# Optimization experiments

Measured on AMD Instinct MI355X. Metric: run time of the kernel, lower is better.

## Reference

```python
import jax, jax.numpy as jnp
import numpy as np

N_NODES = 50000
N_EDGES = 600000
D = 128
R = 8


def setup_inputs() -> dict:
    key = jax.random.key(0)
    ks = jax.random.split(key, 10)
    return {
        "node_ids": jnp.arange(N_NODES, dtype=jnp.int32),
        "src": jax.random.randint(ks[0], (N_EDGES,), 0, N_NODES, dtype=jnp.int32),
        "dst": jax.random.randint(ks[1], (N_EDGES,), 0, N_NODES, dtype=jnp.int32),
        "etype": jax.random.randint(ks[2], (N_EDGES,), 0, R, dtype=jnp.int32),
        "emb": jax.random.normal(ks[3], (N_NODES, D), dtype=jnp.float32) * 0.02,
        "W1": jax.random.normal(ks[4], (R, D, D), dtype=jnp.float32) * 0.05,
        "Wself1": jax.random.normal(ks[5], (D, D), dtype=jnp.float32) * 0.05,
        "b1": jnp.zeros((D,), dtype=jnp.float32),
        "W2": jax.random.normal(ks[6], (R, D, D), dtype=jnp.float32) * 0.05,
        "Wself2": jax.random.normal(ks[7], (D, D), dtype=jnp.float32) * 0.05,
        "b2": jnp.zeros((D,), dtype=jnp.float32),
    }


def rgcn_layer(h, W, Wself, b, src, dst, etype, n_nodes):
    # relation-wise transform of all node features: [R, N, d_out]
    hr = jnp.einsum('nd,rdo->rno', h, W)
    # per-edge gather of (relation, src) -> message, then scatter-sum to dst
    msgs = hr[etype, src]                                   # [E, d_out]
    agg = jax.ops.segment_sum(msgs, dst, num_segments=n_nodes)
    # self-loop + bias (activation=None, feat_drop=0)
    return agg + h @ Wself + b


def reference(node_ids, src, dst, etype, emb, W1, Wself1, b1, W2, Wself2, b2):
    h0 = emb[node_ids]                                      # embedding lookup over all nodes
    h1 = rgcn_layer(h0, W1, Wself1, b1, src, dst, etype, emb.shape[0])
    h2 = rgcn_layer(h1, W2, Wself2, b2, src, dst, etype, emb.shape[0])
    return h2
```

## Files before the change

kernel.cpp:

```cpp
#include <hip/hip_runtime.h>
#include <hip/hip_bf16.h>

#define NN 50000
#define NE 600000
#define DD 128
#define NR 8
#define NB (NN * NR)
#define NCHUNK8 ((NB + 255) / 256)
#define PERT ((NCHUNK8 + 255) / 256)
#define CAPE 1024

typedef __attribute__((ext_vector_type(8))) short bf16x8;
typedef __attribute__((ext_vector_type(4))) float f32x4;

__device__ __forceinline__ unsigned short f2bf(float f) {
  __hip_bfloat16 h = __float2bfloat16(f);
  return *reinterpret_cast<unsigned short*>(&h);
}
__device__ __forceinline__ unsigned pk2(float lo, float hi) {
  return (unsigned)f2bf(lo) | ((unsigned)f2bf(hi) << 16);
}
__device__ __forceinline__ float bflo(unsigned u) { return __uint_as_float(u << 16); }
__device__ __forceinline__ float bfhi(unsigned u) { return __uint_as_float(u & 0xffff0000u); }

__global__ __launch_bounds__(256) void convw_kernel(
    const float* __restrict__ W1, const float* __restrict__ Ws1,
    const float* __restrict__ W2, const float* __restrict__ Ws2,
    unsigned short* __restrict__ WT)
{
  __shared__ float tile[16][17];
  const int m = blockIdx.y;
  const int t8 = blockIdx.x;
  const int d0 = (t8 >> 3) * 16, o0 = (t8 & 7) * 16;
  const float* src;
  if (m < 8)       src = W1 + (size_t)m * DD * DD;
  else if (m == 8) src = Ws1;
  else if (m < 17) src = W2 + (size_t)(m - 9) * DD * DD;
  else             src = Ws2;
  const int tx = threadIdx.x & 15, ty = threadIdx.x >> 4;
  tile[ty][tx] = src[(size_t)(d0 + ty) * DD + o0 + tx];
  __syncthreads();
  WT[(size_t)m * DD * DD + (o0 + ty) * DD + d0 + tx] = f2bf(tile[tx][ty]);
}

__global__ __launch_bounds__(256) void convh_kernel(
    const float* __restrict__ emb, const int* __restrict__ ids,
    unsigned short* __restrict__ h)
{
  const int gid = blockIdx.x * 256 + threadIdx.x;
  if (gid >= NN * 16) return;
  const int row = gid >> 4;
  const int off = (gid & 15) * 8;
  const int srcRow = ids[row];
  const float* src = emb + (size_t)srcRow * DD + off;
  const float4 a = *reinterpret_cast<const float4*>(src);
  const float4 b = *reinterpret_cast<const float4*>(src + 4);
  uint4 u;
  u.x = pk2(a.x, a.y); u.y = pk2(a.z, a.w);
  u.z = pk2(b.x, b.y); u.w = pk2(b.z, b.w);
  *reinterpret_cast<uint4*>(h + (size_t)row * DD + off) = u;
}

__global__ __launch_bounds__(256) void hist_kernel(
    const int* __restrict__ dst, const int* __restrict__ et,
    int* __restrict__ deg)
{
  const int e = blockIdx.x * 256 + threadIdx.x;
  if (e < NE) atomicAdd(&deg[dst[e] * NR + et[e]], 1);
}

__global__ __launch_bounds__(256) void bsum_kernel(
    const int* __restrict__ deg, int* __restrict__ bsum)
{
  __shared__ int tmp[256];
  const int t = threadIdx.x;
  const int i = blockIdx.x * 256 + t;
  tmp[t] = (i < NB) ? deg[i] : 0;
  __syncthreads();
#pragma unroll
  for (int off = 128; off > 0; off >>= 1) {
    if (t < off) tmp[t] += tmp[t + off];
    __syncthreads();
  }
  if (t == 0) bsum[blockIdx.x] = tmp[0];
}

__global__ __launch_bounds__(256) void bscan_kernel(
    const int* __restrict__ bsum, int* __restrict__ bbase)
{
  __shared__ int tmp[256];
  const int t = threadIdx.x;
  const int b = t * PERT;
  const int e = min(b + PERT, NCHUNK8);
  int s = 0;
  for (int i = b; i < e; ++i) s += bsum[i];
  tmp[t] = s;
  __syncthreads();
#pragma unroll
  for (int off = 1; off < 256; off <<= 1) {
    const int x = (t >= off) ? tmp[t - off] : 0;
    __syncthreads();
    tmp[t] += x;
    __syncthreads();
  }
  int run = tmp[t] - s;
  for (int i = b; i < e; ++i) {
    const int v = bsum[i];
    bbase[i] = run;
    run += v;
  }
}

__global__ __launch_bounds__(256) void expand_kernel(
    int* deg, const int* __restrict__ bbase, int* __restrict__ offsets)
{
  __shared__ int tmp[256];
  const int t = threadIdx.x;
  const int i = blockIdx.x * 256 + t;
  const int v = (i < NB) ? deg[i] : 0;
  tmp[t] = v;
  __syncthreads();
#pragma unroll
  for (int off = 1; off < 256; off <<= 1) {
    const int x = (t >= off) ? tmp[t - off] : 0;
    __syncthreads();
    tmp[t] += x;
    __syncthreads();
  }
  const int base = bbase[blockIdx.x];
  const int excl = base + tmp[t] - v;
  if (i < NB) {
    offsets[i] = excl;
    deg[i] = excl;
    if (i == NB - 1) offsets[NB] = base + tmp[t];
  }
}

__global__ __launch_bounds__(256) void fill_kernel(
    const int* __restrict__ src, const int* __restrict__ dst,
    const int* __restrict__ et, int* __restrict__ cursor,
    int* __restrict__ eidx)
{
  const int e = blockIdx.x * 256 + threadIdx.x;
  if (e < NE) {
    const int pos = atomicAdd(&cursor[dst[e] * NR + et[e]], 1);
    eidx[pos] = src[e];
  }
}

__device__ __forceinline__ void gather_frag_lds(
    const unsigned short* __restrict__ h,
    const int* __restrict__ eidx, const int* ldsE, int blockBeg,
    int beg, int end, int g, bf16x8* frag)
{
  float s[4][8];
#pragma unroll
  for (int ks = 0; ks < 4; ++ks)
#pragma unroll
    for (int j = 0; j < 8; ++j) s[ks][j] = 0.f;
  for (int i = beg; i < end; ++i) {
    const int li = i - blockBeg;
    const int idx = (li < CAPE) ? ldsE[li] : eidx[i];
    const unsigned short* hp = h + (size_t)idx * DD + g * 8;
#pragma unroll
    for (int ks = 0; ks < 4; ++ks) {
      const uint4 q = *reinterpret_cast<const uint4*>(hp + ks * 32);
      s[ks][0] += bflo(q.x); s[ks][1] += bfhi(q.x);
      s[ks][2] += bflo(q.y); s[ks][3] += bfhi(q.y);
      s[ks][4] += bflo(q.z); s[ks][5] += bfhi(q.z);
      s[ks][6] += bflo(q.w); s[ks][7] += bfhi(q.w);
    }
  }
#pragma unroll
  for (int ks = 0; ks < 4; ++ks) {
    uint4 u;
    u.x = pk2(s[ks][0], s[ks][1]);
    u.y = pk2(s[ks][2], s[ks][3]);
    u.z = pk2(s[ks][4], s[ks][5]);
    u.w = pk2(s[ks][6], s[ks][7]);
    frag[ks] = *reinterpret_cast<bf16x8*>(&u);
  }
}

template<int OUTF32>
__global__ __launch_bounds__(256, 4) void layer_kernel(
    const unsigned short* __restrict__ h,
    const int* __restrict__ off8, const int* __restrict__ eidx,
    const unsigned short* __restrict__ WTl,
    const float* __restrict__ bias,
    void* __restrict__ out)
{
  __shared__ __align__(16) char ldsW[2][DD * 64 * 2];
  __shared__ int ldsO[64 * NR + 1];
  __shared__ int ldsE[CAPE];

  const int tid = threadIdx.x;
  const int rowBase = blockIdx.x * 64;
  const int lane = tid & 63;
  const int w = tid >> 6;
  const int c = lane & 15;
  const int g = lane >> 4;
  const int n = rowBase + w * 16 + c;
  const int nld = (n < NN) ? n : (NN - 1);
  const int lnode = nld - rowBase;

  const int nNodes = (NN - rowBase < 64) ? (NN - rowBase) : 64;
  const int onum = nNodes * NR + 1;
  for (int i = tid; i < onum; i += 256) ldsO[i] = off8[rowBase * NR + i];
  __syncthreads();
  const int blockBeg = ldsO[0];
  const int blockCnt = ldsO[onum - 1] - blockBeg;
  const int stCnt = (blockCnt < CAPE) ? blockCnt : CAPE;
  for (int i = tid; i < stCnt; i += 256) ldsE[i] = eidx[blockBeg + i];

  int dstB[4], srcRel[4];
#pragma unroll
  for (int j = 0; j < 4; ++j) {
    const int i = tid + j * 256;
    const int o = i >> 3, slot = i & 7;
    dstB[j] = ((o << 7) | (slot << 4)) ^ ((o & 7) << 4);
    srcRel[j] = o * DD + slot * 8;
  }

  uint4 wreg[4];
#pragma unroll
  for (int j = 0; j < 4; ++j)
    wreg[j] = *reinterpret_cast<const uint4*>(WTl + srcRel[j]);
#pragma unroll
  for (int j = 0; j < 4; ++j)
    *reinterpret_cast<uint4*>(ldsW[0] + dstB[j]) = wreg[j];
  __syncthreads();

  bf16x8 fA[4], fB[4];
  gather_frag_lds(h, eidx, ldsE, blockBeg, ldsO[lnode * NR], ldsO[lnode * NR + 1], g, fA);

  f32x4 acc[8];
#pragma unroll
  for (int t = 0; t < 8; ++t) acc[t] = (f32x4){0.f, 0.f, 0.f, 0.f};

#define PH(P, CUR, NXT)                                                               \
  {                                                                                   \
    __syncthreads();                                                                  \
    if ((P) < 17) {                                                                   \
      const unsigned short* wsrc = WTl                                                \
          + (size_t)(((P) + 1) >> 1) * DD * DD + (((P) + 1) & 1) * 64;                \
      _Pragma("unroll")                                                               \
      for (int j = 0; j < 4; ++j)                                                     \
        wreg[j] = *reinterpret_cast<const uint4*>(wsrc + srcRel[j]);                  \
    }                                                                                 \
    int gb = 0, ge = 0;                                                               \
    if (((P) & 1) == 0 && ((P) >> 1) + 1 < NR) {                                      \
      const int lo = lnode * NR + ((P) >> 1) + 1;                                     \
      gb = ldsO[lo]; ge = ldsO[lo + 1];                                               \
    }                                                                                 \
    _Pragma("unroll")                                                                 \
    for (int kl = 0; kl < 2; ++kl) {                                                  \
      _Pragma("unroll")                                                               \
      for (int t = 0; t < 8; ++t) {                                                   \
        const int addr = (((t * 16 + c) << 7) + ((kl * 4 + g) << 4)) ^ ((c & 7) << 4); \
        bf16x8 a = *reinterpret_cast<const bf16x8*>(ldsW[(P) & 1] + addr);            \
        acc[t] = __builtin_amdgcn_mfma_f32_16x16x32_bf16(                             \
            a, CUR[((P) & 1) * 2 + kl], acc[t], 0, 0, 0);                             \
      }                                                                               \
    }                                                                                 \
    if (((P) & 1) == 0) {                                                             \
      if (((P) >> 1) + 1 < NR) {                                                      \
        gather_frag_lds(h, eidx, ldsE, blockBeg, gb, ge, g, NXT);                     \
      } else if (((P) >> 1) + 1 == NR) {                                              \
        _Pragma("unroll")                                                             \
        for (int ks = 0; ks < 4; ++ks)                                                \
          NXT[ks] = *reinterpret_cast<const bf16x8*>(                                 \
              h + (size_t)nld * DD + ks * 32 + g * 8);                                \
      }                                                                               \
    }                                                                                 \
    if ((P) < 17) {                                                                   \
      _Pragma("unroll")                                                               \
      for (int j = 0; j < 4; ++j)                                                     \
        *reinterpret_cast<uint4*>(ldsW[((P) + 1) & 1] + dstB[j]) = wreg[j];           \
    }                                                                                 \
  }

  PH(0, fA, fB)  PH(1, fA, fB)
  PH(2, fB, fA)  PH(3, fB, fA)
  PH(4, fA, fB)  PH(5, fA, fB)
  PH(6, fB, fA)  PH(7, fB, fA)
  PH(8, fA, fB)  PH(9, fA, fB)
  PH(10, fB, fA) PH(11, fB, fA)
  PH(12, fA, fB) PH(13, fA, fB)
  PH(14, fB, fA) PH(15, fB, fA)
  PH(16, fA, fB) PH(17, fA, fB)
#undef PH

  if (n >= NN) return;
  if (OUTF32) {
    float* dst = (float*)out + (size_t)n * DD;
#pragma unroll
    for (int t = 0; t < 8; ++t) {
      const int o0 = t * 16 + g * 4;
      const float4 bv = *reinterpret_cast<const float4*>(bias + o0);
      float4 o;
      o.x = acc[t][0] + bv.x; o.y = acc[t][1] + bv.y;
      o.z = acc[t][2] + bv.z; o.w = acc[t][3] + bv.w;
      *reinterpret_cast<float4*>(dst + o0) = o;
    }
  } else {
    unsigned short* dst = (unsigned short*)out + (size_t)n * DD;
#pragma unroll
    for (int t = 0; t < 8; ++t) {
      const int o0 = t * 16 + g * 4;
      const float4 bv = *reinterpret_cast<const float4*>(bias + o0);
      uint2 q;
      q.x = pk2(acc[t][0] + bv.x, acc[t][1] + bv.y);
      q.y = pk2(acc[t][2] + bv.z, acc[t][3] + bv.w);
      *reinterpret_cast<uint2*>(dst + o0) = q;
    }
  }
}

extern "C" void kernel_launch(void* const* d_in, const int* in_sizes, int n_in,
                              void* d_out, int out_size, void* d_ws, size_t ws_size,
                              hipStream_t stream) {
  const int*   node_ids = (const int*)d_in[0];
  const int*   src   = (const int*)d_in[1];
  const int*   dst   = (const int*)d_in[2];
  const int*   etype = (const int*)d_in[3];
  const float* emb   = (const float*)d_in[4];
  const float* W1    = (const float*)d_in[5];
  const float* Ws1   = (const float*)d_in[6];
  const float* b1    = (const float*)d_in[7];
  const float* W2    = (const float*)d_in[8];
  const float* Ws2   = (const float*)d_in[9];
  const float* b2    = (const float*)d_in[10];

  char* p = (char*)d_ws;
  unsigned short* h0 = (unsigned short*)p;  p += (size_t)NN * DD * 2;
  unsigned short* h1 = (unsigned short*)p;  p += (size_t)NN * DD * 2;
  unsigned short* WT = (unsigned short*)p;  p += (size_t)18 * DD * DD * 2;
  int* off8          = (int*)p;             p += (size_t)(NB + 1) * 4;
  int* deg8          = (int*)p;             p += (size_t)NB * 4;
  int* eidx          = (int*)p;             p += (size_t)NE * 4;
  int* bsum          = (int*)p;             p += (size_t)NCHUNK8 * 4;
  int* bbase         = (int*)p;

  const int eb = (NE + 255) / 256;
  const int tb = (NN + 63) / 64;

  convw_kernel<<<dim3(64, 18), 256, 0, stream>>>(W1, Ws1, W2, Ws2, WT);
  convh_kernel<<<(NN * 16) / 256, 256, 0, stream>>>(emb, node_ids, h0);
  hipMemsetAsync(deg8, 0, (size_t)NB * 4, stream);
  hist_kernel<<<eb, 256, 0, stream>>>(dst, etype, deg8);
  bsum_kernel<<<NCHUNK8, 256, 0, stream>>>(deg8, bsum);
  bscan_kernel<<<1, 256, 0, stream>>>(bsum, bbase);
  expand_kernel<<<NCHUNK8, 256, 0, stream>>>(deg8, bbase, off8);
  fill_kernel<<<eb, 256, 0, stream>>>(src, dst, etype, deg8, eidx);

  layer_kernel<0><<<tb, 256, 0, stream>>>(h0, off8, eidx, WT, b1, h1);
  layer_kernel<1><<<tb, 256, 0, stream>>>(h1, off8, eidx, WT + (size_t)9 * DD * DD, b2, (float*)d_out);
}
```

Before: 238.4 us.

## Fuse CSR build and conversion kernels into one cooperative grid-sync kernel

```diff
diff --git a/kernel.cpp b/kernel.cpp
--- a/kernel.cpp
+++ b/kernel.cpp
@@ -1,5 +1,8 @@
 #include <hip/hip_runtime.h>
 #include <hip/hip_bf16.h>
+#include <hip/hip_cooperative_groups.h>
+
+namespace cg = cooperative_groups;
 
 #define NN 50000
 #define NE 600000
@@ -9,6 +12,7 @@
 #define NCHUNK8 ((NB + 255) / 256)
 #define PERT ((NCHUNK8 + 255) / 256)
 #define CAPE 1024
+#define COOPB 1024
 
 typedef __attribute__((ext_vector_type(8))) short bf16x8;
 typedef __attribute__((ext_vector_type(4))) float f32x4;
@@ -23,128 +27,129 @@
 __device__ __forceinline__ float bflo(unsigned u) { return __uint_as_float(u << 16); }
 __device__ __forceinline__ float bfhi(unsigned u) { return __uint_as_float(u & 0xffff0000u); }
 
-__global__ __launch_bounds__(256) void convw_kernel(
+__global__ __launch_bounds__(256) void csr_coop_kernel(
     const float* __restrict__ W1, const float* __restrict__ Ws1,
     const float* __restrict__ W2, const float* __restrict__ Ws2,
-    unsigned short* __restrict__ WT)
+    const float* __restrict__ emb, const int* __restrict__ ids,
+    const int* __restrict__ srcA, const int* __restrict__ dstA,
+    const int* __restrict__ etA,
+    unsigned short* __restrict__ WT, unsigned short* __restrict__ h0,
+    int* deg, int* off8, int* __restrict__ eidx,
+    int* __restrict__ bsum, int* __restrict__ bbase)
 {
+  cg::grid_group grid = cg::this_grid();
   __shared__ float tile[16][17];
-  const int m = blockIdx.y;
-  const int t8 = blockIdx.x;
-  const int d0 = (t8 >> 3) * 16, o0 = (t8 & 7) * 16;
-  const float* src;
-  if (m < 8)       src = W1 + (size_t)m * DD * DD;
-  else if (m == 8) src = Ws1;
-  else if (m < 17) src = W2 + (size_t)(m - 9) * DD * DD;
-  else             src = Ws2;
-  const int tx = threadIdx.x & 15, ty = threadIdx.x >> 4;
-  tile[ty][tx] = src[(size_t)(d0 + ty) * DD + o0 + tx];
-  __syncthreads();
-  WT[(size_t)m * DD * DD + (o0 + ty) * DD + d0 + tx] = f2bf(tile[tx][ty]);
-}
-
-__global__ __launch_bounds__(256) void convh_kernel(
-    const float* __restrict__ emb, const int* __restrict__ ids,
-    unsigned short* __restrict__ h)
-{
-  const int gid = blockIdx.x * 256 + threadIdx.x;
-  if (gid >= NN * 16) return;
-  const int row = gid >> 4;
-  const int off = (gid & 15) * 8;
-  const int srcRow = ids[row];
-  const float* src = emb + (size_t)srcRow * DD + off;
-  const float4 a = *reinterpret_cast<const float4*>(src);
-  const float4 b = *reinterpret_cast<const float4*>(src + 4);
-  uint4 u;
-  u.x = pk2(a.x, a.y); u.y = pk2(a.z, a.w);
-  u.z = pk2(b.x, b.y); u.w = pk2(b.z, b.w);
-  *reinterpret_cast<uint4*>(h + (size_t)row * DD + off) = u;
-}
-
-__global__ __launch_bounds__(256) void hist_kernel(
-    const int* __restrict__ dst, const int* __restrict__ et,
-    int* __restrict__ deg)
-{
-  const int e = blockIdx.x * 256 + threadIdx.x;
-  if (e < NE) atomicAdd(&deg[dst[e] * NR + et[e]], 1);
-}
-
-__global__ __launch_bounds__(256) void bsum_kernel(
-    const int* __restrict__ deg, int* __restrict__ bsum)
-{
   __shared__ int tmp[256];
+
   const int t = threadIdx.x;
-  const int i = blockIdx.x * 256 + t;
-  tmp[t] = (i < NB) ? deg[i] : 0;
-  __syncthreads();
-#pragma unroll
-  for (int off = 128; off > 0; off >>= 1) {
-    if (t < off) tmp[t] += tmp[t + off];
-    __syncthreads();
-  }
-  if (t == 0) bsum[blockIdx.x] = tmp[0];
-}
-
-__global__ __launch_bounds__(256) void bscan_kernel(
-    const int* __restrict__ bsum, int* __restrict__ bbase)
-{
-  __shared__ int tmp[256];
-  const int t = threadIdx.x;
-  const int b = t * PERT;
-  const int e = min(b + PERT, NCHUNK8);
-  int s = 0;
-  for (int i = b; i < e; ++i) s += bsum[i];
-  tmp[t] = s;
-  __syncthreads();
-#pragma unroll
-  for (int off = 1; off < 256; off <<= 1) {
-    const int x = (t >= off) ? tmp[t - off] : 0;
-    __syncthreads();
-    tmp[t] += x;
-    __syncthreads();
-  }
-  int run = tmp[t] - s;
-  for (int i = b; i < e; ++i) {
-    const int v = bsum[i];
-    bbase[i] = run;
-    run += v;
-  }
-}
-
-__global__ __launch_bounds__(256) void expand_kernel(
-    int* deg, const int* __restrict__ bbase, int* __restrict__ offsets)
-{
-  __shared__ int tmp[256];
-  const int t = threadIdx.x;
-  const int i = blockIdx.x * 256 + t;
-  const int v = (i < NB) ? deg[i] : 0;
-  tmp[t] = v;
-  __syncthreads();
-#pragma unroll
-  for (int off = 1; off < 256; off <<= 1) {
-    const int x = (t >= off) ? tmp[t - off] : 0;
-    __syncthreads();
-    tmp[t] += x;
-    __syncthreads();
-  }
-  const int base = bbase[blockIdx.x];
-  const int excl = base + tmp[t] - v;
-  if (i < NB) {
-    offsets[i] = excl;
-    deg[i] = excl;
-    if (i == NB - 1) offsets[NB] = base + tmp[t];
-  }
-}
-
-__global__ __launch_bounds__(256) void fill_kernel(
-    const int* __restrict__ src, const int* __restrict__ dst,
-    const int* __restrict__ et, int* __restrict__ cursor,
-    int* __restrict__ eidx)
-{
-  const int e = blockIdx.x * 256 + threadIdx.x;
-  if (e < NE) {
-    const int pos = atomicAdd(&cursor[dst[e] * NR + et[e]], 1);
-    eidx[pos] = src[e];
+  const int b = blockIdx.x;
+  const int nthr = COOPB * 256;
+  const int gid0 = b * 256 + t;
+  const int tx = t & 15, ty = t >> 4;
+
+  for (int tileId = b; tileId < 18 * 64; tileId += COOPB) {
+    const int m = tileId >> 6, t8 = tileId & 63;
+    const int d0 = (t8 >> 3) * 16, o0 = (t8 & 7) * 16;
+    const float* sw;
+    if (m < 8)       sw = W1 + (size_t)m * DD * DD;
+    else if (m == 8) sw = Ws1;
+    else if (m < 17) sw = W2 + (size_t)(m - 9) * DD * DD;
+    else             sw = Ws2;
+    __syncthreads();
+    tile[ty][tx] = sw[(size_t)(d0 + ty) * DD + o0 + tx];
+    __syncthreads();
+    WT[(size_t)m * DD * DD + (o0 + ty) * DD + d0 + tx] = f2bf(tile[tx][ty]);
+  }
+
+  for (int gid = gid0; gid < NN * 16; gid += nthr) {
+    const int row = gid >> 4;
+    const int off = (gid & 15) * 8;
+    const int srcRow = ids[row];
+    const float* s = emb + (size_t)srcRow * DD + off;
+    const float4 a = *reinterpret_cast<const float4*>(s);
+    const float4 c = *reinterpret_cast<const float4*>(s + 4);
+    uint4 u;
+    u.x = pk2(a.x, a.y); u.y = pk2(a.z, a.w);
+    u.z = pk2(c.x, c.y); u.w = pk2(c.z, c.w);
+    *reinterpret_cast<uint4*>(h0 + (size_t)row * DD + off) = u;
+  }
+
+  for (int i = gid0; i < NB; i += nthr) deg[i] = 0;
+
+  grid.sync();
+
+  for (int e = gid0; e < NE; e += nthr)
+    atomicAdd(&deg[dstA[e] * NR + etA[e]], 1);
+
+  grid.sync();
+
+  for (int ch = b; ch < NCHUNK8; ch += COOPB) {
+    const int i = ch * 256 + t;
+    __syncthreads();
+    tmp[t] = (i < NB) ? deg[i] : 0;
+    __syncthreads();
+#pragma unroll
+    for (int off = 128; off > 0; off >>= 1) {
+      if (t < off) tmp[t] += tmp[t + off];
+      __syncthreads();
+    }
+    if (t == 0) bsum[ch] = tmp[0];
+  }
+
+  grid.sync();
+
+  if (b == 0) {
+    const int bb = t * PERT;
+    const int ee = min(bb + PERT, NCHUNK8);
+    int s = 0;
+    for (int i = bb; i < ee; ++i) s += bsum[i];
+    __syncthreads();
+    tmp[t] = s;
+    __syncthreads();
+#pragma unroll
+    for (int off = 1; off < 256; off <<= 1) {
+      const int x = (t >= off) ? tmp[t - off] : 0;
+      __syncthreads();
+      tmp[t] += x;
+      __syncthreads();
+    }
+    int run = tmp[t] - s;
+    for (int i = bb; i < ee; ++i) {
+      const int v = bsum[i];
+      bbase[i] = run;
+      run += v;
+    }
+  }
+
+  grid.sync();
+
+  for (int ch = b; ch < NCHUNK8; ch += COOPB) {
+    const int i = ch * 256 + t;
+    const int v = (i < NB) ? deg[i] : 0;
+    __syncthreads();
+    tmp[t] = v;
+    __syncthreads();
+#pragma unroll
+    for (int off = 1; off < 256; off <<= 1) {
+      const int x = (t >= off) ? tmp[t - off] : 0;
+      __syncthreads();
+      tmp[t] += x;
+      __syncthreads();
+    }
+    const int base = bbase[ch];
+    const int excl = base + tmp[t] - v;
+    if (i < NB) {
+      off8[i] = excl;
+      deg[i] = excl;
+      if (i == NB - 1) off8[NB] = base + tmp[t];
+    }
+  }
+
+  grid.sync();
+
+  for (int e = gid0; e < NE; e += nthr) {
+    const int pos = atomicAdd(&deg[dstA[e] * NR + etA[e]], 1);
+    eidx[pos] = srcA[e];
   }
 }
 
@@ -342,17 +347,20 @@
   int* bsum          = (int*)p;             p += (size_t)NCHUNK8 * 4;
   int* bbase         = (int*)p;
 
-  const int eb = (NE + 255) / 256;
   const int tb = (NN + 63) / 64;
 
-  convw_kernel<<<dim3(64, 18), 256, 0, stream>>>(W1, Ws1, W2, Ws2, WT);
-  convh_kernel<<<(NN * 16) / 256, 256, 0, stream>>>(emb, node_ids, h0);
-  hipMemsetAsync(deg8, 0, (size_t)NB * 4, stream);
-  hist_kernel<<<eb, 256, 0, stream>>>(dst, etype, deg8);
-  bsum_kernel<<<NCHUNK8, 256, 0, stream>>>(deg8, bsum);
-  bscan_kernel<<<1, 256, 0, stream>>>(bsum, bbase);
-  expand_kernel<<<NCHUNK8, 256, 0, stream>>>(deg8, bbase, off8);
-  fill_kernel<<<eb, 256, 0, stream>>>(src, dst, etype, deg8, eidx);
+  {
+    void* args[] = {
+      (void*)&W1, (void*)&Ws1, (void*)&W2, (void*)&Ws2,
+      (void*)&emb, (void*)&node_ids,
+      (void*)&src, (void*)&dst, (void*)&etype,
+      (void*)&WT, (void*)&h0,
+      (void*)&deg8, (void*)&off8, (void*)&eidx,
+      (void*)&bsum, (void*)&bbase
+    };
+    hipLaunchCooperativeKernel((void*)csr_coop_kernel,
+                               dim3(COOPB), dim3(256), args, 0, stream);
+  }
 
   layer_kernel<0><<<tb, 256, 0, stream>>>(h0, off8, eidx, WT, b1, h1);
   layer_kernel<1><<<tb, 256, 0, stream>>>(h1, off8, eidx, WT + (size_t)9 * DD * DD, b2, (float*)d_out);
```

Measured after the change: 762.4 us. 220% more time.

## Split relation reduction across two block groups with a separate combine pass

Applied to the files above, without the earlier changes.

```diff
diff --git a/kernel.cpp b/kernel.cpp
--- a/kernel.cpp
+++ b/kernel.cpp
@@ -182,19 +182,18 @@
   }
 }
 
-template<int OUTF32>
-__global__ __launch_bounds__(256, 4) void layer_kernel(
+__global__ __launch_bounds__(256, 4) void layer_split_kernel(
     const unsigned short* __restrict__ h,
     const int* __restrict__ off8, const int* __restrict__ eidx,
     const unsigned short* __restrict__ WTl,
-    const float* __restrict__ bias,
-    void* __restrict__ out)
+    float* __restrict__ pA, float* __restrict__ pB)
 {
   __shared__ __align__(16) char ldsW[2][DD * 64 * 2];
   __shared__ int ldsO[64 * NR + 1];
   __shared__ int ldsE[CAPE];
 
   const int tid = threadIdx.x;
+  const int grp = blockIdx.y;
   const int rowBase = blockIdx.x * 64;
   const int lane = tid & 63;
   const int w = tid >> 6;
@@ -203,6 +202,7 @@
   const int n = rowBase + w * 16 + c;
   const int nld = (n < NN) ? n : (NN - 1);
   const int lnode = nld - rowBase;
+  const int nph = grp ? 8 : 10;
 
   const int nNodes = (NN - rowBase < 64) ? (NN - rowBase) : 64;
   const int onum = nNodes * NR + 1;
@@ -222,35 +222,45 @@
     srcRel[j] = o * DD + slot * 8;
   }
 
+#define MATOF(i) (grp ? (4 + (i)) : (((i) < 4) ? (i) : 8))
+
   uint4 wreg[4];
-#pragma unroll
-  for (int j = 0; j < 4; ++j)
-    wreg[j] = *reinterpret_cast<const uint4*>(WTl + srcRel[j]);
+  {
+    const unsigned short* wsrc = WTl + (size_t)MATOF(0) * DD * DD;
+#pragma unroll
+    for (int j = 0; j < 4; ++j)
+      wreg[j] = *reinterpret_cast<const uint4*>(wsrc + srcRel[j]);
+  }
 #pragma unroll
   for (int j = 0; j < 4; ++j)
     *reinterpret_cast<uint4*>(ldsW[0] + dstB[j]) = wreg[j];
   __syncthreads();
 
   bf16x8 fA[4], fB[4];
-  gather_frag_lds(h, eidx, ldsE, blockBeg, ldsO[lnode * NR], ldsO[lnode * NR + 1], g, fA);
+  {
+    const int r0 = grp ? 4 : 0;
+    gather_frag_lds(h, eidx, ldsE, blockBeg,
+                    ldsO[lnode * NR + r0], ldsO[lnode * NR + r0 + 1], g, fA);
+  }
 
   f32x4 acc[8];
 #pragma unroll
   for (int t = 0; t < 8; ++t) acc[t] = (f32x4){0.f, 0.f, 0.f, 0.f};
 
 #define PH(P, CUR, NXT)                                                               \
-  {                                                                                   \
+  if ((P) < nph) {                                                                    \
     __syncthreads();                                                                  \
-    if ((P) < 17) {                                                                   \
+    if ((P) + 1 < nph) {                                                              \
       const unsigned short* wsrc = WTl                                                \
-          + (size_t)(((P) + 1) >> 1) * DD * DD + (((P) + 1) & 1) * 64;                \
+          + (size_t)MATOF(((P) + 1) >> 1) * DD * DD + (((P) + 1) & 1) * 64;           \
       _Pragma("unroll")                                                               \
       for (int j = 0; j < 4; ++j)                                                     \
         wreg[j] = *reinterpret_cast<const uint4*>(wsrc + srcRel[j]);                  \
     }                                                                                 \
     int gb = 0, ge = 0;                                                               \
-    if (((P) & 1) == 0 && ((P) >> 1) + 1 < NR) {                                      \
-      const int lo = lnode * NR + ((P) >> 1) + 1;                                     \
+    const int rn = ((P) >> 1) + 1;                                                    \
+    if (((P) & 1) == 0 && rn < 4) {                                                   \
+      const int lo = lnode * NR + (grp ? 4 : 0) + rn;                                 \
       gb = ldsO[lo]; ge = ldsO[lo + 1];                                               \
     }                                                                                 \
     _Pragma("unroll")                                                                 \
@@ -264,16 +274,16 @@
       }                                                                               \
     }                                                                                 \
     if (((P) & 1) == 0) {                                                             \
-      if (((P) >> 1) + 1 < NR) {                                                      \
+      if (rn < 4) {                                                                   \
         gather_frag_lds(h, eidx, ldsE, blockBeg, gb, ge, g, NXT);                     \
-      } else if (((P) >> 1) + 1 == NR) {                                              \
+      } else if (rn == 4 && grp == 0) {                                               \
         _Pragma("unroll")                                                             \
         for (int ks = 0; ks < 4; ++ks)                                                \
           NXT[ks] = *reinterpret_cast<const bf16x8*>(                                 \
               h + (size_t)nld * DD + ks * 32 + g * 8);                                \
       }                                                                               \
     }                                                                                 \
-    if ((P) < 17) {                                                                   \
+    if ((P) + 1 < nph) {                                                              \
       _Pragma("unroll")                                                               \
       for (int j = 0; j < 4; ++j)                                                     \
         *reinterpret_cast<uint4*>(ldsW[((P) + 1) & 1] + dstB[j]) = wreg[j];           \
@@ -285,35 +295,37 @@
   PH(4, fA, fB)  PH(5, fA, fB)
   PH(6, fB, fA)  PH(7, fB, fA)
   PH(8, fA, fB)  PH(9, fA, fB)
-  PH(10, fB, fA) PH(11, fB, fA)
-  PH(12, fA, fB) PH(13, fA, fB)
-  PH(14, fB, fA) PH(15, fB, fA)
-  PH(16, fA, fB) PH(17, fA, fB)
 #undef PH
+#undef MATOF
 
   if (n >= NN) return;
+  float* pout = (grp ? pB : pA) + (size_t)n * DD;
+#pragma unroll
+  for (int t = 0; t < 8; ++t)
+    *reinterpret_cast<f32x4*>(pout + t * 16 + g * 4) = acc[t];
+}
+
+template<int OUTF32>
+__global__ __launch_bounds__(256) void combine_kernel(
+    const float* __restrict__ pA, const float* __restrict__ pB,
+    const float* __restrict__ bias, void* __restrict__ out)
+{
+  const int i = blockIdx.x * 256 + threadIdx.x;
+  if (i >= NN * DD / 4) return;
+  const float4 a = reinterpret_cast<const float4*>(pA)[i];
+  const float4 b = reinterpret_cast<const float4*>(pB)[i];
+  const int col = (i * 4) & (DD - 1);
+  const float4 bv = *reinterpret_cast<const float4*>(bias + col);
+  float4 o;
+  o.x = a.x + b.x + bv.x; o.y = a.y + b.y + bv.y;
+  o.z = a.z + b.z + bv.z; o.w = a.w + b.w + bv.w;
   if (OUTF32) {
-    float* dst = (float*)out + (size_t)n * DD;
-#pragma unroll
-    for (int t = 0; t < 8; ++t) {
-      const int o0 = t * 16 + g * 4;
-      const float4 bv = *reinterpret_cast<const float4*>(bias + o0);
-      float4 o;
-      o.x = acc[t][0] + bv.x; o.y = acc[t][1] + bv.y;
-      o.z = acc[t][2] + bv.z; o.w = acc[t][3] + bv.w;
-      *reinterpret_cast<float4*>(dst + o0) = o;
-    }
+    reinterpret_cast<float4*>(out)[i] = o;
   } else {
-    unsigned short* dst = (unsigned short*)out + (size_t)n * DD;
-#pragma unroll
-    for (int t = 0; t < 8; ++t) {
-      const int o0 = t * 16 + g * 4;
-      const float4 bv = *reinterpret_cast<const float4*>(bias + o0);
-      uint2 q;
-      q.x = pk2(acc[t][0] + bv.x, acc[t][1] + bv.y);
-      q.y = pk2(acc[t][2] + bv.z, acc[t][3] + bv.w);
-      *reinterpret_cast<uint2*>(dst + o0) = q;
-    }
+    uint2 q;
+    q.x = pk2(o.x, o.y);
+    q.y = pk2(o.z, o.w);
+    reinterpret_cast<uint2*>(out)[i] = q;
   }
 }
 
@@ -340,10 +352,13 @@
   int* deg8          = (int*)p;             p += (size_t)NB * 4;
   int* eidx          = (int*)p;             p += (size_t)NE * 4;
   int* bsum          = (int*)p;             p += (size_t)NCHUNK8 * 4;
-  int* bbase         = (int*)p;
+  int* bbase         = (int*)p;             p += (size_t)NCHUNK8 * 4;
+  float* pA          = (float*)p;           p += (size_t)NN * DD * 4;
+  float* pB          = (float*)p;
 
   const int eb = (NE + 255) / 256;
   const int tb = (NN + 63) / 64;
+  const int cb = (NN * DD / 4 + 255) / 256;
 
   convw_kernel<<<dim3(64, 18), 256, 0, stream>>>(W1, Ws1, W2, Ws2, WT);
   convh_kernel<<<(NN * 16) / 256, 256, 0, stream>>>(emb, node_ids, h0);
@@ -354,6 +369,8 @@
   expand_kernel<<<NCHUNK8, 256, 0, stream>>>(deg8, bbase, off8);
   fill_kernel<<<eb, 256, 0, stream>>>(src, dst, etype, deg8, eidx);
 
-  layer_kernel<0><<<tb, 256, 0, stream>>>(h0, off8, eidx, WT, b1, h1);
-  layer_kernel<1><<<tb, 256, 0, stream>>>(h1, off8, eidx, WT + (size_t)9 * DD * DD, b2, (float*)d_out);
-}
+  layer_split_kernel<<<dim3(tb, 2), 256, 0, stream>>>(h0, off8, eidx, WT, pA, pB);
+  combine_kernel<0><<<cb, 256, 0, stream>>>(pA, pB, b1, h1);
+  layer_split_kernel<<<dim3(tb, 2), 256, 0, stream>>>(h1, off8, eidx, WT + (size_t)9 * DD * DD, pA, pB);
+  combine_kernel<1><<<cb, 256, 0, stream>>>(pA, pB, b2, (float*)d_out);
+}
```

New measurement: 322.1 us. +35.1%, slower.
